# Performance work log

Measured on AMD Instinct MI355X. Metric: run time of the kernel, lower is better.

## Reference

```python
import jax, jax.numpy as jnp
import numpy as np

N, F, H, D, E, G = 50000, 64, 4, 64, 800000, 64
NEG_SLOPE = 0.2


def setup_inputs() -> dict:
    key = jax.random.key(0)
    ks = jax.random.split(key, 10)
    return {
        "x": jax.random.normal(ks[0], (N, F), jnp.float32),
        "mask": jax.random.uniform(ks[1], (N, F), jnp.float32),
        "edge_index": jax.random.randint(ks[2], (2, E), 0, N, jnp.int64),
        "batch_idx": jnp.sort(jax.random.randint(ks[3], (N,), 0, G, jnp.int64)),
        "W_gat": jax.random.normal(ks[4], (H * D, F), jnp.float32) * 0.05,
        "att_src": jax.random.normal(ks[5], (H, D), jnp.float32) * 0.05,
        "att_dst": jax.random.normal(ks[6], (H, D), jnp.float32) * 0.05,
        "bias_gat": jax.random.normal(ks[7], (H * D,), jnp.float32) * 0.05,
        "W_lin": jax.random.normal(ks[8], (D, H * D), jnp.float32) * 0.05,
        "b_lin": jax.random.normal(ks[9], (D,), jnp.float32) * 0.05,
    }


def reference(x, mask, edge_index, batch_idx, W_gat, att_src, att_dst, bias_gat, W_lin, b_lin):
    n = x.shape[0]
    row, col = edge_index[0], edge_index[1]

    # ---- get_mask(mask, edge_index, hops=1): scatter_add(mask[col] -> row), threshold
    m = jax.ops.segment_sum(mask[col], row, num_segments=n)
    m = (m > 0).astype(x.dtype)  # [N, F]

    # ---- GATConv(x, edge_index): add self loops (PyG default)
    loop = jnp.arange(n, dtype=edge_index.dtype)
    src = jnp.concatenate([edge_index[0], loop])  # source j
    dst = jnp.concatenate([edge_index[1], loop])  # target i

    xw = (x @ W_gat.T).reshape(n, H, D)  # per-head projection [N,H,D]
    a_s = jnp.einsum("nhd,hd->nh", xw, att_src)  # [N,H]
    a_d = jnp.einsum("nhd,hd->nh", xw, att_dst)
    e = jax.nn.leaky_relu(a_s[src] + a_d[dst], NEG_SLOPE)  # [E+N, H]

    # segment softmax over incoming edges of each destination node
    emax = jax.ops.segment_max(e, dst, num_segments=n)  # [N,H]
    ex = jnp.exp(e - emax[dst])
    denom = jax.ops.segment_sum(ex, dst, num_segments=n)
    alpha = ex / (denom[dst] + 1e-16)  # [E+N, H]

    out = jax.ops.segment_sum(alpha[:, :, None] * xw[src], dst, num_segments=n)
    out = out.reshape(n, H * D) + bias_gat  # concat heads + bias

    # ---- mask expand to heads and fuse: x = linear(x * mask)
    mexp = jnp.broadcast_to(m[:, None, :], (n, H, F)).reshape(n, H * F)
    out = (out * mexp) @ W_lin.T + b_lin  # [N, D]

    # ---- GraphSizeNorm: divide by sqrt(#nodes in each graph)
    deg = jax.ops.segment_sum(jnp.ones((n,), x.dtype), batch_idx, num_segments=G)
    inv_sqrt = jnp.where(deg > 0, deg, 1.0) ** -0.5
    out = out * inv_sqrt[batch_idx][:, None]
    return out
```

## Files before the change

kernel.cpp:

```cpp
#include <hip/hip_runtime.h>
#include <cstdint>
#include <math.h>

constexpr float NEG_SLOPE = 0.2f;

__device__ __forceinline__ float lrelu(float v) { return v > 0.0f ? v : NEG_SLOPE * v; }

__device__ __forceinline__ unsigned short f2bf(float f) {
    uint32_t u = __float_as_uint(f);
    uint32_t r = (u + 0x7fffu + ((u >> 16) & 1u)) >> 16;
    return (unsigned short)r;
}
__device__ __forceinline__ float bf2f(unsigned short v) { return __uint_as_float((uint32_t)v << 16); }
__device__ __forceinline__ float bflo(uint32_t v) { return __uint_as_float(v << 16); }
__device__ __forceinline__ float bfhi(uint32_t v) { return __uint_as_float(v & 0xffff0000u); }

typedef short bf16x8 __attribute__((ext_vector_type(8)));
typedef float f32x4 __attribute__((ext_vector_type(4)));

__global__ void k_init(const float* __restrict__ mask,
                       unsigned long long* __restrict__ mbits,
                       unsigned long long* __restrict__ magg,
                       int* __restrict__ deg, int* __restrict__ startg, int N)
{
    if (blockIdx.x == 0 && threadIdx.x < 64) startg[threadIdx.x] = N;
    int wid  = (blockIdx.x * blockDim.x + threadIdx.x) >> 6;
    int lane = threadIdx.x & 63;
    if (wid >= N) return;
    float v = mask[(size_t)wid * 64 + lane];
    unsigned long long b = __ballot(v > 0.0f);
    if (lane == 0) { mbits[wid] = b; magg[wid] = 0ULL; deg[wid] = 0; }
}

__global__ void k_deg(const int* __restrict__ ei, int* __restrict__ deg, int E)
{
    int e = blockIdx.x * blockDim.x + threadIdx.x;
    if (e >= E) return;
    atomicAdd(deg + ei[E + e], 1);
}

__launch_bounds__(256)
__global__ void k_att2(const float* __restrict__ x, const float* __restrict__ Wg,
                       const float* __restrict__ att_s, const float* __restrict__ att_d,
                       float* __restrict__ a_s, float* __restrict__ a_d, int N)
{
    __shared__ float vs_l[256];
    __shared__ float vd_l[256];
    int tid = threadIdx.x;
    {
        int h = tid >> 6, k = tid & 63;
        float s = 0.f, d = 0.f;
        for (int dd = 0; dd < 64; ++dd) {
            float w = Wg[(size_t)(h * 64 + dd) * 64 + k];
            s += w * att_s[h * 64 + dd];
            d += w * att_d[h * 64 + dd];
        }
        vs_l[tid] = s; vd_l[tid] = d;
    }
    __syncthreads();
    int i = blockIdx.x * 256 + tid;
    if (i >= N) return;
    const float4* xr = (const float4*)(x + (size_t)i * 64);
    float s0=0,s1=0,s2=0,s3=0, d0=0,d1=0,d2=0,d3=0;
    #pragma unroll
    for (int q = 0; q < 16; ++q) {
        float4 xv = xr[q];
        float4 a0 = *(const float4*)&vs_l[4*q];
        float4 a1 = *(const float4*)&vs_l[64 + 4*q];
        float4 a2 = *(const float4*)&vs_l[128 + 4*q];
        float4 a3 = *(const float4*)&vs_l[192 + 4*q];
        float4 c0 = *(const float4*)&vd_l[4*q];
        float4 c1 = *(const float4*)&vd_l[64 + 4*q];
        float4 c2 = *(const float4*)&vd_l[128 + 4*q];
        float4 c3 = *(const float4*)&vd_l[192 + 4*q];
        s0 += xv.x*a0.x + xv.y*a0.y + xv.z*a0.z + xv.w*a0.w;
        s1 += xv.x*a1.x + xv.y*a1.y + xv.z*a1.z + xv.w*a1.w;
        s2 += xv.x*a2.x + xv.y*a2.y + xv.z*a2.z + xv.w*a2.w;
        s3 += xv.x*a3.x + xv.y*a3.y + xv.z*a3.z + xv.w*a3.w;
        d0 += xv.x*c0.x + xv.y*c0.y + xv.z*c0.z + xv.w*c0.w;
        d1 += xv.x*c1.x + xv.y*c1.y + xv.z*c1.z + xv.w*c1.w;
        d2 += xv.x*c2.x + xv.y*c2.y + xv.z*c2.z + xv.w*c2.w;
        d3 += xv.x*c3.x + xv.y*c3.y + xv.z*c3.z + xv.w*c3.w;
    }
    *(float4*)&a_s[(size_t)i * 4] = make_float4(s0, s1, s2, s3);
    *(float4*)&a_d[(size_t)i * 4] = make_float4(d0, d1, d2, d3);
}

__launch_bounds__(256)
__global__ void k_gemm1m(const float* __restrict__ x, const float* __restrict__ Wg,
                         const int* __restrict__ batch_idx,
                         uint32_t* __restrict__ xwp, int* __restrict__ startg, int N)
{
    __shared__ __align__(16) uint32_t AsH[2048];
    __shared__ __align__(16) uint32_t AsL[2048];
    __shared__ __align__(16) uint32_t BsH[8192];
    const int tid = threadIdx.x;
    const int r0  = blockIdx.x * 64;

    for (int idx = tid; idx < 2048; idx += 256) {
        int r = idx >> 5, k2 = idx & 31;
        float2 v = make_float2(0.f, 0.f);
        if (r0 + r < N) v = *(const float2*)&x[(size_t)(r0 + r) * 64 + 2 * k2];
        unsigned short h0 = f2bf(v.x), h1 = f2bf(v.y);
        unsigned short l0 = f2bf(v.x - bf2f(h0)), l1 = f2bf(v.y - bf2f(h1));
        int di = (r * 32 + k2) ^ ((r & 7) << 2);
        AsH[di] = (uint32_t)h0 | ((uint32_t)h1 << 16);
        AsL[di] = (uint32_t)l0 | ((uint32_t)l1 << 16);
    }
    for (int idx = tid; idx < 8192; idx += 256) {
        int c = idx >> 5, k2 = idx & 31;
        float2 v = *(const float2*)&Wg[(size_t)c * 64 + 2 * k2];
        int di = (c * 32 + k2) ^ ((c & 7) << 2);
        BsH[di] = (uint32_t)f2bf(v.x) | ((uint32_t)f2bf(v.y) << 16);
    }
    if (tid < 64 && (r0 + tid) < N) {
        int i = r0 + tid;
        int b = batch_idx[i];
        int pb = (i > 0) ? batch_idx[i - 1] : -1;
        if (b != pb) startg[b] = i;
    }
    __syncthreads();

    const int lane = tid & 63;
    const int wv   = tid >> 6;
    const int rl   = lane & 15;
    const int kg   = lane >> 4;
    const int ct0  = (wv & 1) * 2 + (wv >> 1) * 8;
    const int swz  = (rl & 7) << 2;

    f32x4 acc[4][4];
    #pragma unroll
    for (int r = 0; r < 4; ++r)
        #pragma unroll
        for (int cs = 0; cs < 4; ++cs) acc[r][cs] = (f32x4){0.f, 0.f, 0.f, 0.f};

    #pragma unroll
    for (int ks = 0; ks < 2; ++ks) {
        bf16x8 aH[4], aL[4], bH[4];
        #pragma unroll
        for (int r = 0; r < 4; ++r) {
            int ui = (((r * 16 + rl) * 32) + ks * 16 + kg * 4) ^ swz;
            aH[r] = *(const bf16x8*)&AsH[ui];
            aL[r] = *(const bf16x8*)&AsL[ui];
        }
        #pragma unroll
        for (int cs = 0; cs < 4; ++cs) {
            int ct = ct0 + (cs & 1) + (cs >> 1) * 4;
            int ui = (((ct * 16 + rl) * 32) + ks * 16 + kg * 4) ^ swz;
            bH[cs] = *(const bf16x8*)&BsH[ui];
        }
        #pragma unroll
        for (int r = 0; r < 4; ++r)
            #pragma unroll
            for (int cs = 0; cs < 4; ++cs) {
                acc[r][cs] = __builtin_amdgcn_mfma_f32_16x16x32_bf16(aH[r], bH[cs], acc[r][cs], 0, 0, 0);
                acc[r][cs] = __builtin_amdgcn_mfma_f32_16x16x32_bf16(aL[r], bH[cs], acc[r][cs], 0, 0, 0);
            }
    }

    #pragma unroll
    for (int r = 0; r < 4; ++r) {
        #pragma unroll
        for (int reg = 0; reg < 4; ++reg) {
            int row = r0 + r * 16 + kg * 4 + reg;
            if (row < N) {
                #pragma unroll
                for (int p = 0; p < 2; ++p) {
                    int c_lo = (ct0 + p) * 16 + rl;
                    int wrd  = ((c_lo >> 7) << 6) | (c_lo & 63);
                    uint32_t lo = f2bf(acc[r][p][reg]);
                    uint32_t hi = f2bf(acc[r][p + 2][reg]);
                    xwp[(size_t)row * 128 + wrd] = lo | (hi << 16);
                }
            }
        }
    }
}

__global__ void k_scan1(const int* __restrict__ deg, int* __restrict__ off,
                        int* __restrict__ bsum, int N)
{
    __shared__ int s[256];
    int t = threadIdx.x;
    int i = blockIdx.x * 256 + t;
    int v = (i < N) ? deg[i] : 0;
    s[t] = v; __syncthreads();
    for (int o = 1; o < 256; o <<= 1) {
        int u = (t >= o) ? s[t - o] : 0;
        __syncthreads();
        s[t] += u;
        __syncthreads();
    }
    int incl = s[t];
    if (i < N) off[i] = incl - v;
    if (t == 255) bsum[blockIdx.x] = incl;
}

__global__ void k_scan2(const int* __restrict__ bsum, int* __restrict__ bpre,
                        int* __restrict__ off, const int* __restrict__ startg,
                        float* __restrict__ invs, int NB, int N)
{
    __shared__ int s[256];
    int t = threadIdx.x;
    int v = (t < NB) ? bsum[t] : 0;
    s[t] = v; __syncthreads();
    for (int o = 1; o < 256; o <<= 1) {
        int u = (t >= o) ? s[t - o] : 0;
        __syncthreads();
        s[t] += u;
        __syncthreads();
    }
    if (t < NB) bpre[t] = s[t] - v;
    if (t == 255) off[N] = s[255];
    if (t < 64) {
        int st = startg[t];
        int en = N;
        for (int g2 = t + 1; g2 < 64; ++g2) en = min(en, startg[g2]);
        int d = en - st;
        float dv = (d > 0) ? (float)d : 1.0f;
        invs[t] = 1.0f / sqrtf(dv);
    }
}

__global__ void k_scan3(int* __restrict__ off, int* __restrict__ cursor,
                        const int* __restrict__ bpre, int N)
{
    int i = blockIdx.x * blockDim.x + threadIdx.x;
    if (i >= N) return;
    int v = off[i] + bpre[blockIdx.x];
    off[i] = v;
    cursor[i] = v;
}

__global__ void k_fill(const int* __restrict__ ei, int* __restrict__ cursor,
                       int* __restrict__ csr,
                       const unsigned long long* __restrict__ mbits,
                       unsigned long long* __restrict__ magg, int E)
{
    int e = blockIdx.x * blockDim.x + threadIdx.x;
    if (e >= E) return;
    int r = ei[e];
    int c = ei[E + e];
    unsigned long long b = mbits[c];
    if ((magg[r] & b) != b) atomicOr(magg + r, b);
    int pos = atomicAdd(cursor + c, 1);
    csr[pos] = r;
}

__launch_bounds__(256)
__global__ void k_main6(const uint32_t* __restrict__ xwp,
                        const float* __restrict__ a_s,
                        const float* __restrict__ a_d,
                        const int* __restrict__ off,
                        const int* __restrict__ csr,
                        const unsigned long long* __restrict__ magg,
                        const float* __restrict__ bias,
                        float* __restrict__ tb, int N)
{
    __shared__ __align__(16) uint32_t su[4][64];
    __shared__ __align__(16) float2 e01s[4][64];
    __shared__ __align__(16) float2 e23s[4][64];

    const int lane = threadIdx.x & 63;
    const int wv   = threadIdx.x >> 6;
    const int wid  = blockIdx.x * 4 + wv;
    const int nw   = gridDim.x * 4;
    const int hp   = lane >> 5;
    const int d0   = (lane & 31) * 2;

    const uint2* xw2 = (const uint2*)xwp;
    const float2 bsL = *(const float2*)&bias[hp * 128 + d0];
    const float2 bsH = *(const float2*)&bias[hp * 128 + 64 + d0];
    const float2* ep = hp ? e23s[wv] : e01s[wv];

    for (int i = wid; i < N; i += nw) {
        const int beg = off[i], end = off[i + 1];
        const float4 adv = *(const float4*)(a_d + (size_t)i * 4);
        const float4 asv = *(const float4*)(a_s + (size_t)i * 4);
        const float ex0 = __expf(lrelu(asv.x + adv.x));
        const float ex1 = __expf(lrelu(asv.y + adv.y));
        const float ex2 = __expf(lrelu(asv.z + adv.z));
        const float ex3 = __expf(lrelu(asv.w + adv.w));

        const uint2 sv = xw2[(size_t)i * 64 + lane];
        const float wls = hp ? ex2 : ex0;
        const float whs = hp ? ex3 : ex1;
        float accL0 = wls * bflo(sv.x), accH0 = whs * bfhi(sv.x);
        float accL1 = wls * bflo(sv.y), accH1 = whs * bfhi(sv.y);
        float s0 = 0.f, s1 = 0.f, s2 = 0.f, s3 = 0.f;

        for (int kc = beg; kc < end; kc += 64) {
            const int cnt = min(64, end - kc);
            uint32_t sreg = 0; float e0 = 0.f, e1 = 0.f, e2 = 0.f, e3 = 0.f;
            if (lane < cnt) {
                sreg = csr[kc + lane];
                const float4 g = *(const float4*)(a_s + (size_t)sreg * 4);
                e0 = __expf(lrelu(g.x + adv.x));
                e1 = __expf(lrelu(g.y + adv.y));
                e2 = __expf(lrelu(g.z + adv.z));
                e3 = __expf(lrelu(g.w + adv.w));
            }
            s0 += e0; s1 += e1; s2 += e2; s3 += e3;
            su[wv][lane]   = sreg;
            e01s[wv][lane] = make_float2(e0, e1);
            e23s[wv][lane] = make_float2(e2, e3);

            int j = 0;
            for (; j + 8 <= cnt; j += 8) {
                uint4 sq0 = *(const uint4*)&su[wv][j];
                uint4 sq1 = *(const uint4*)&su[wv][j + 4];
                float2 w0 = ep[j],   w1 = ep[j+1], w2 = ep[j+2], w3 = ep[j+3];
                float2 w4 = ep[j+4], w5 = ep[j+5], w6 = ep[j+6], w7 = ep[j+7];
                uint2 v0 = xw2[(size_t)sq0.x * 64 + lane];
                uint2 v1 = xw2[(size_t)sq0.y * 64 + lane];
                uint2 v2 = xw2[(size_t)sq0.z * 64 + lane];
                uint2 v3 = xw2[(size_t)sq0.w * 64 + lane];
                uint2 v4 = xw2[(size_t)sq1.x * 64 + lane];
                uint2 v5 = xw2[(size_t)sq1.y * 64 + lane];
                uint2 v6 = xw2[(size_t)sq1.z * 64 + lane];
                uint2 v7 = xw2[(size_t)sq1.w * 64 + lane];
                accL0 += w0.x * bflo(v0.x); accH0 += w0.y * bfhi(v0.x);
                accL1 += w0.x * bflo(v0.y); accH1 += w0.y * bfhi(v0.y);
                accL0 += w1.x * bflo(v1.x); accH0 += w1.y * bfhi(v1.x);
                accL1 += w1.x * bflo(v1.y); accH1 += w1.y * bfhi(v1.y);
                accL0 += w2.x * bflo(v2.x); accH0 += w2.y * bfhi(v2.x);
                accL1 += w2.x * bflo(v2.y); accH1 += w2.y * bfhi(v2.y);
                accL0 += w3.x * bflo(v3.x); accH0 += w3.y * bfhi(v3.x);
                accL1 += w3.x * bflo(v3.y); accH1 += w3.y * bfhi(v3.y);
                accL0 += w4.x * bflo(v4.x); accH0 += w4.y * bfhi(v4.x);
                accL1 += w4.x * bflo(v4.y); accH1 += w4.y * bfhi(v4.y);
                accL0 += w5.x * bflo(v5.x); accH0 += w5.y * bfhi(v5.x);
                accL1 += w5.x * bflo(v5.y); accH1 += w5.y * bfhi(v5.y);
                accL0 += w6.x * bflo(v6.x); accH0 += w6.y * bfhi(v6.x);
                accL1 += w6.x * bflo(v6.y); accH1 += w6.y * bfhi(v6.y);
                accL0 += w7.x * bflo(v7.x); accH0 += w7.y * bfhi(v7.x);
                accL1 += w7.x * bflo(v7.y); accH1 += w7.y * bfhi(v7.y);
            }
            for (; j + 4 <= cnt; j += 4) {
                uint4 sq = *(const uint4*)&su[wv][j];
                float2 wA = ep[j], wB = ep[j+1], wC = ep[j+2], wD = ep[j+3];
                uint2 vA = xw2[(size_t)sq.x * 64 + lane];
                uint2 vB = xw2[(size_t)sq.y * 64 + lane];
                uint2 vC = xw2[(size_t)sq.z * 64 + lane];
                uint2 vD = xw2[(size_t)sq.w * 64 + lane];
                accL0 += wA.x * bflo(vA.x); accH0 += wA.y * bfhi(vA.x);
                accL1 += wA.x * bflo(vA.y); accH1 += wA.y * bfhi(vA.y);
                accL0 += wB.x * bflo(vB.x); accH0 += wB.y * bfhi(vB.x);
                accL1 += wB.x * bflo(vB.y); accH1 += wB.y * bfhi(vB.y);
                accL0 += wC.x * bflo(vC.x); accH0 += wC.y * bfhi(vC.x);
                accL1 += wC.x * bflo(vC.y); accH1 += wC.y * bfhi(vC.y);
                accL0 += wD.x * bflo(vD.x); accH0 += wD.y * bfhi(vD.x);
                accL1 += wD.x * bflo(vD.y); accH1 += wD.y * bfhi(vD.y);
            }
            for (; j < cnt; ++j) {
                uint32_t s = su[wv][j];
                float2 wE = ep[j];
                uint2 v = xw2[(size_t)s * 64 + lane];
                accL0 += wE.x * bflo(v.x); accH0 += wE.y * bfhi(v.x);
                accL1 += wE.x * bflo(v.y); accH1 += wE.y * bfhi(v.y);
            }
        }
        #pragma unroll
        for (int o = 1; o < 64; o <<= 1) {
            s0 += __shfl_xor(s0, o); s1 += __shfl_xor(s1, o);
            s2 += __shfl_xor(s2, o); s3 += __shfl_xor(s3, o);
        }
        s0 += ex0; s1 += ex1; s2 += ex2; s3 += ex3;
        const float slo = hp ? s2 : s0;
        const float shi = hp ? s3 : s1;
        const float rlo = 1.0f / (slo + 1e-16f);
        const float rhi = 1.0f / (shi + 1e-16f);

        const unsigned long long mb = magg[i];
        const float m0 = (float)((mb >> d0) & 1ULL);
        const float m1 = (float)((mb >> (d0 + 1)) & 1ULL);
        float2 oL = make_float2((accL0 * rlo + bsL.x) * m0, (accL1 * rlo + bsL.y) * m1);
        float2 oH = make_float2((accH0 * rhi + bsH.x) * m0, (accH1 * rhi + bsH.y) * m1);
        *(float2*)&tb[(size_t)i * 256 + hp * 128 + d0]      = oL;
        *(float2*)&tb[(size_t)i * 256 + hp * 128 + 64 + d0] = oH;
    }
}

__launch_bounds__(256)
__global__ void k_gemm2m(const float* __restrict__ tb, const float* __restrict__ Wl,
                         const float* __restrict__ bl,
                         const int* __restrict__ batch_idx, const float* __restrict__ invs,
                         float* __restrict__ out, int N)
{
    __shared__ __align__(16) uint32_t AH[2048];
    __shared__ __align__(16) uint32_t AL[2048];
    __shared__ __align__(16) uint32_t BH[2048];
    __shared__ __align__(16) uint32_t BL[2048];
    const int tid = threadIdx.x;
    const int r0  = blockIdx.x * 64;
    const int lane = tid & 63;
    const int wv   = tid >> 6;
    const int rl   = lane & 15;
    const int kg   = lane >> 4;
    const int swz  = (rl & 7) << 2;

    f32x4 acc[4];
    #pragma unroll
    for (int r = 0; r < 4; ++r) acc[r] = (f32x4){0.f, 0.f, 0.f, 0.f};

    for (int kc = 0; kc < 4; ++kc) {
        if (kc) __syncthreads();
        for (int idx = tid; idx < 2048; idx += 256) {
            int r = idx >> 5, k2 = idx & 31;
            float2 v = make_float2(0.f, 0.f);
            if (r0 + r < N) v = *(const float2*)&tb[(size_t)(r0 + r) * 256 + kc * 64 + 2 * k2];
            unsigned short h0 = f2bf(v.x), h1 = f2bf(v.y);
            unsigned short l0 = f2bf(v.x - bf2f(h0)), l1 = f2bf(v.y - bf2f(h1));
            int di = (r * 32 + k2) ^ ((r & 7) << 2);
            AH[di] = (uint32_t)h0 | ((uint32_t)h1 << 16);
            AL[di] = (uint32_t)l0 | ((uint32_t)l1 << 16);
        }
        for (int idx = tid; idx < 2048; idx += 256) {
            int c = idx >> 5, k2 = idx & 31;
            float2 v = *(const float2*)&Wl[(size_t)c * 256 + kc * 64 + 2 * k2];
            unsigned short h0 = f2bf(v.x), h1 = f2bf(v.y);
            unsigned short l0 = f2bf(v.x - bf2f(h0)), l1 = f2bf(v.y - bf2f(h1));
            int di = (c * 32 + k2) ^ ((c & 7) << 2);
            BH[di] = (uint32_t)h0 | ((uint32_t)h1 << 16);
            BL[di] = (uint32_t)l0 | ((uint32_t)l1 << 16);
        }
        __syncthreads();

        #pragma unroll
        for (int ks = 0; ks < 2; ++ks) {
            int uib = ((wv * 16 + rl) * 32 + ks * 16 + kg * 4) ^ swz;
            bf16x8 bHf = *(const bf16x8*)&BH[uib];
            bf16x8 bLf = *(const bf16x8*)&BL[uib];
            #pragma unroll
            for (int r = 0; r < 4; ++r) {
                int ui = ((r * 16 + rl) * 32 + ks * 16 + kg * 4) ^ swz;
                bf16x8 aHf = *(const bf16x8*)&AH[ui];
                bf16x8 aLf = *(const bf16x8*)&AL[ui];
                acc[r] = __builtin_amdgcn_mfma_f32_16x16x32_bf16(aHf, bHf, acc[r], 0, 0, 0);
                acc[r] = __builtin_amdgcn_mfma_f32_16x16x32_bf16(aHf, bLf, acc[r], 0, 0, 0);
                acc[r] = __builtin_amdgcn_mfma_f32_16x16x32_bf16(aLf, bHf, acc[r], 0, 0, 0);
            }
        }
    }

    const int col = wv * 16 + rl;
    const float blc = bl[col];
    #pragma unroll
    for (int r = 0; r < 4; ++r) {
        #pragma unroll
        for (int reg = 0; reg < 4; ++reg) {
            int row = r0 + r * 16 + kg * 4 + reg;
            if (row < N) {
                float sc = invs[batch_idx[row]];
                out[(size_t)row * 64 + col] = (acc[r][reg] + blc) * sc;
            }
        }
    }
}

extern "C" void kernel_launch(void* const* d_in, const int* in_sizes, int n_in,
                              void* d_out, int out_size, void* d_ws, size_t ws_size,
                              hipStream_t stream)
{
    const float* x      = (const float*)d_in[0];
    const float* mask   = (const float*)d_in[1];
    const int*   ei     = (const int*)d_in[2];
    const int*   batch  = (const int*)d_in[3];
    const float* Wg     = (const float*)d_in[4];
    const float* att_s  = (const float*)d_in[5];
    const float* att_d  = (const float*)d_in[6];
    const float* bias_g = (const float*)d_in[7];
    const float* Wl     = (const float*)d_in[8];
    const float* bl     = (const float*)d_in[9];
    float* out = (float*)d_out;

    const int N = in_sizes[0] / 64;
    const int E = in_sizes[2] / 2;

    char* w = (char*)d_ws;
    auto alloc = [&](size_t bytes) { char* p = w; w += (bytes + 255) & ~(size_t)255; return p; };
    uint32_t* xwp  = (uint32_t*)alloc((size_t)N * 128 * 4);
    float* tbuf  = (float*)alloc((size_t)N * 256 * 4);
    float* a_s   = (float*)alloc((size_t)N * 4 * 4);
    float* a_d   = (float*)alloc((size_t)N * 4 * 4);
    unsigned long long* mbits = (unsigned long long*)alloc((size_t)N * 8);
    unsigned long long* magg  = (unsigned long long*)alloc((size_t)N * 8);
    int* deg    = (int*)alloc((size_t)N * 4);
    int* off    = (int*)alloc((size_t)(N + 1) * 4);
    int* cursor = (int*)alloc((size_t)N * 4);
    int* csr    = (int*)alloc((size_t)E * 4);
    int* bsum   = (int*)alloc(256 * 4);
    int* bpre   = (int*)alloc(256 * 4);
    int* startg = (int*)alloc(64 * 4);
    float* invs = (float*)alloc(64 * 4);

    int nbN4  = (N + 3) / 4;
    int nb256 = (N + 255) / 256;

    k_init<<<nbN4, 256, 0, stream>>>(mask, mbits, magg, deg, startg, N);
    k_deg<<<(E + 255) / 256, 256, 0, stream>>>(ei, deg, E);
    k_att2<<<nb256, 256, 0, stream>>>(x, Wg, att_s, att_d, a_s, a_d, N);
    k_gemm1m<<<(N + 63) / 64, 256, 0, stream>>>(x, Wg, batch, xwp, startg, N);
    k_scan1<<<nb256, 256, 0, stream>>>(deg, off, bsum, N);
    k_scan2<<<1, 256, 0, stream>>>(bsum, bpre, off, startg, invs, nb256, N);
    k_scan3<<<nb256, 256, 0, stream>>>(off, cursor, bpre, N);
    k_fill<<<(E + 255) / 256, 256, 0, stream>>>(ei, cursor, csr, mbits, magg, E);
    k_main6<<<2048, 256, 0, stream>>>(xwp, a_s, a_d, off, csr, magg, bias_g, tbuf, N);
    k_gemm2m<<<(N + 63) / 64, 256, 0, stream>>>(tbuf, Wl, bl, batch, invs, out, N);
}
```

Baseline: 243.5 us.

## Store attention output as bf16, fuse init kernels, drop softmax-sum shuffles

The GAT aggregation kernel now writes its per-node output as packed bf16 instead of fp32. This halves the intermediate buffer traffic and lets the second GEMM skip the hi/lo split of A and one of its three MFMAs. The zero-init of deg/magg/startg moves into the attention-score kernel, and the mask-ballot and degree-count kernels merge into one launch. The softmax denominators are now accumulated per lane from the shared weights, replacing the cross-lane shuffle reduction. The bf16 intermediate trades accuracy for bandwidth.

```diff
diff --git a/kernel.cpp b/kernel.cpp
--- a/kernel.cpp
+++ b/kernel.cpp
@@ -18,31 +18,12 @@
 typedef short bf16x8 __attribute__((ext_vector_type(8)));
 typedef float f32x4 __attribute__((ext_vector_type(4)));
 
-__global__ void k_init(const float* __restrict__ mask,
-                       unsigned long long* __restrict__ mbits,
-                       unsigned long long* __restrict__ magg,
-                       int* __restrict__ deg, int* __restrict__ startg, int N)
-{
-    if (blockIdx.x == 0 && threadIdx.x < 64) startg[threadIdx.x] = N;
-    int wid  = (blockIdx.x * blockDim.x + threadIdx.x) >> 6;
-    int lane = threadIdx.x & 63;
-    if (wid >= N) return;
-    float v = mask[(size_t)wid * 64 + lane];
-    unsigned long long b = __ballot(v > 0.0f);
-    if (lane == 0) { mbits[wid] = b; magg[wid] = 0ULL; deg[wid] = 0; }
-}
-
-__global__ void k_deg(const int* __restrict__ ei, int* __restrict__ deg, int E)
-{
-    int e = blockIdx.x * blockDim.x + threadIdx.x;
-    if (e >= E) return;
-    atomicAdd(deg + ei[E + e], 1);
-}
-
 __launch_bounds__(256)
-__global__ void k_att2(const float* __restrict__ x, const float* __restrict__ Wg,
-                       const float* __restrict__ att_s, const float* __restrict__ att_d,
-                       float* __restrict__ a_s, float* __restrict__ a_d, int N)
+__global__ void k_att2z(const float* __restrict__ x, const float* __restrict__ Wg,
+                        const float* __restrict__ att_s, const float* __restrict__ att_d,
+                        float* __restrict__ a_s, float* __restrict__ a_d,
+                        int* __restrict__ deg, unsigned long long* __restrict__ magg,
+                        int* __restrict__ startg, int N)
 {
     __shared__ float vs_l[256];
     __shared__ float vd_l[256];
@@ -57,9 +38,11 @@
         }
         vs_l[tid] = s; vd_l[tid] = d;
     }
+    if (blockIdx.x == 0 && tid < 64) startg[tid] = N;
     __syncthreads();
     int i = blockIdx.x * 256 + tid;
     if (i >= N) return;
+    deg[i] = 0; magg[i] = 0ULL;
     const float4* xr = (const float4*)(x + (size_t)i * 64);
     float s0=0,s1=0,s2=0,s3=0, d0=0,d1=0,d2=0,d3=0;
     #pragma unroll
@@ -86,6 +69,25 @@
     *(float4*)&a_d[(size_t)i * 4] = make_float4(d0, d1, d2, d3);
 }
 
+__global__ void k_maskdeg(const float* __restrict__ mask, const int* __restrict__ ei,
+                          unsigned long long* __restrict__ mbits, int* __restrict__ deg,
+                          int N, int E, int nbMask)
+{
+    int tid = threadIdx.x;
+    if ((int)blockIdx.x < nbMask) {
+        int wid  = (blockIdx.x * 256 + tid) >> 6;
+        int lane = tid & 63;
+        if (wid >= N) return;
+        float v = mask[(size_t)wid * 64 + lane];
+        unsigned long long b = __ballot(v > 0.0f);
+        if (lane == 0) mbits[wid] = b;
+    } else {
+        int e = (blockIdx.x - nbMask) * 256 + tid;
+        if (e >= E) return;
+        atomicAdd(deg + ei[E + e], 1);
+    }
+}
+
 __launch_bounds__(256)
 __global__ void k_gemm1m(const float* __restrict__ x, const float* __restrict__ Wg,
                          const int* __restrict__ batch_idx,
@@ -248,14 +250,14 @@
 }
 
 __launch_bounds__(256)
-__global__ void k_main6(const uint32_t* __restrict__ xwp,
+__global__ void k_main7(const uint32_t* __restrict__ xwp,
                         const float* __restrict__ a_s,
                         const float* __restrict__ a_d,
                         const int* __restrict__ off,
                         const int* __restrict__ csr,
                         const unsigned long long* __restrict__ magg,
                         const float* __restrict__ bias,
-                        float* __restrict__ tb, int N)
+                        uint32_t* __restrict__ tbp, int N)
 {
     __shared__ __align__(16) uint32_t su[4][64];
     __shared__ __align__(16) float2 e01s[4][64];
@@ -287,7 +289,7 @@
         const float whs = hp ? ex3 : ex1;
         float accL0 = wls * bflo(sv.x), accH0 = whs * bfhi(sv.x);
         float accL1 = wls * bflo(sv.y), accH1 = whs * bfhi(sv.y);
-        float s0 = 0.f, s1 = 0.f, s2 = 0.f, s3 = 0.f;
+        float sL = 0.f, sH = 0.f;
 
         for (int kc = beg; kc < end; kc += 64) {
             const int cnt = min(64, end - kc);
@@ -300,7 +302,6 @@
                 e2 = __expf(lrelu(g.z + adv.z));
                 e3 = __expf(lrelu(g.w + adv.w));
             }
-            s0 += e0; s1 += e1; s2 += e2; s3 += e3;
             su[wv][lane]   = sreg;
             e01s[wv][lane] = make_float2(e0, e1);
             e23s[wv][lane] = make_float2(e2, e3);
@@ -319,6 +320,8 @@
                 uint2 v5 = xw2[(size_t)sq1.y * 64 + lane];
                 uint2 v6 = xw2[(size_t)sq1.z * 64 + lane];
                 uint2 v7 = xw2[(size_t)sq1.w * 64 + lane];
+                sL += w0.x + w1.x + w2.x + w3.x + w4.x + w5.x + w6.x + w7.x;
+                sH += w0.y + w1.y + w2.y + w3.y + w4.y + w5.y + w6.y + w7.y;
                 accL0 += w0.x * bflo(v0.x); accH0 += w0.y * bfhi(v0.x);
                 accL1 += w0.x * bflo(v0.y); accH1 += w0.y * bfhi(v0.y);
                 accL0 += w1.x * bflo(v1.x); accH0 += w1.y * bfhi(v1.x);
@@ -343,6 +346,8 @@
                 uint2 vB = xw2[(size_t)sq.y * 64 + lane];
                 uint2 vC = xw2[(size_t)sq.z * 64 + lane];
                 uint2 vD = xw2[(size_t)sq.w * 64 + lane];
+                sL += wA.x + wB.x + wC.x + wD.x;
+                sH += wA.y + wB.y + wC.y + wD.y;
                 accL0 += wA.x * bflo(vA.x); accH0 += wA.y * bfhi(vA.x);
                 accL1 += wA.x * bflo(vA.y); accH1 += wA.y * bfhi(vA.y);
                 accL0 += wB.x * bflo(vB.x); accH0 += wB.y * bfhi(vB.x);
@@ -356,39 +361,31 @@
                 uint32_t s = su[wv][j];
                 float2 wE = ep[j];
                 uint2 v = xw2[(size_t)s * 64 + lane];
+                sL += wE.x; sH += wE.y;
                 accL0 += wE.x * bflo(v.x); accH0 += wE.y * bfhi(v.x);
                 accL1 += wE.x * bflo(v.y); accH1 += wE.y * bfhi(v.y);
             }
         }
-        #pragma unroll
-        for (int o = 1; o < 64; o <<= 1) {
-            s0 += __shfl_xor(s0, o); s1 += __shfl_xor(s1, o);
-            s2 += __shfl_xor(s2, o); s3 += __shfl_xor(s3, o);
-        }
-        s0 += ex0; s1 += ex1; s2 += ex2; s3 += ex3;
-        const float slo = hp ? s2 : s0;
-        const float shi = hp ? s3 : s1;
-        const float rlo = 1.0f / (slo + 1e-16f);
-        const float rhi = 1.0f / (shi + 1e-16f);
+        const float rlo = 1.0f / (sL + wls + 1e-16f);
+        const float rhi = 1.0f / (sH + whs + 1e-16f);
 
         const unsigned long long mb = magg[i];
         const float m0 = (float)((mb >> d0) & 1ULL);
         const float m1 = (float)((mb >> (d0 + 1)) & 1ULL);
-        float2 oL = make_float2((accL0 * rlo + bsL.x) * m0, (accL1 * rlo + bsL.y) * m1);
-        float2 oH = make_float2((accH0 * rhi + bsH.x) * m0, (accH1 * rhi + bsH.y) * m1);
-        *(float2*)&tb[(size_t)i * 256 + hp * 128 + d0]      = oL;
-        *(float2*)&tb[(size_t)i * 256 + hp * 128 + 64 + d0] = oH;
+        float oL0 = (accL0 * rlo + bsL.x) * m0, oL1 = (accL1 * rlo + bsL.y) * m1;
+        float oH0 = (accH0 * rhi + bsH.x) * m0, oH1 = (accH1 * rhi + bsH.y) * m1;
+        tbp[(size_t)i * 128 + hp * 64 + (lane & 31)]      = (uint32_t)f2bf(oL0) | ((uint32_t)f2bf(oL1) << 16);
+        tbp[(size_t)i * 128 + hp * 64 + 32 + (lane & 31)] = (uint32_t)f2bf(oH0) | ((uint32_t)f2bf(oH1) << 16);
     }
 }
 
 __launch_bounds__(256)
-__global__ void k_gemm2m(const float* __restrict__ tb, const float* __restrict__ Wl,
+__global__ void k_gemm2m(const uint32_t* __restrict__ tbp, const float* __restrict__ Wl,
                          const float* __restrict__ bl,
                          const int* __restrict__ batch_idx, const float* __restrict__ invs,
                          float* __restrict__ out, int N)
 {
     __shared__ __align__(16) uint32_t AH[2048];
-    __shared__ __align__(16) uint32_t AL[2048];
     __shared__ __align__(16) uint32_t BH[2048];
     __shared__ __align__(16) uint32_t BL[2048];
     const int tid = threadIdx.x;
@@ -407,13 +404,9 @@
         if (kc) __syncthreads();
         for (int idx = tid; idx < 2048; idx += 256) {
             int r = idx >> 5, k2 = idx & 31;
-            float2 v = make_float2(0.f, 0.f);
-            if (r0 + r < N) v = *(const float2*)&tb[(size_t)(r0 + r) * 256 + kc * 64 + 2 * k2];
-            unsigned short h0 = f2bf(v.x), h1 = f2bf(v.y);
-            unsigned short l0 = f2bf(v.x - bf2f(h0)), l1 = f2bf(v.y - bf2f(h1));
-            int di = (r * 32 + k2) ^ ((r & 7) << 2);
-            AH[di] = (uint32_t)h0 | ((uint32_t)h1 << 16);
-            AL[di] = (uint32_t)l0 | ((uint32_t)l1 << 16);
+            uint32_t v = 0;
+            if (r0 + r < N) v = tbp[(size_t)(r0 + r) * 128 + kc * 32 + k2];
+            AH[(r * 32 + k2) ^ ((r & 7) << 2)] = v;
         }
         for (int idx = tid; idx < 2048; idx += 256) {
             int c = idx >> 5, k2 = idx & 31;
@@ -435,10 +428,8 @@
             for (int r = 0; r < 4; ++r) {
                 int ui = ((r * 16 + rl) * 32 + ks * 16 + kg * 4) ^ swz;
                 bf16x8 aHf = *(const bf16x8*)&AH[ui];
-                bf16x8 aLf = *(const bf16x8*)&AL[ui];
                 acc[r] = __builtin_amdgcn_mfma_f32_16x16x32_bf16(aHf, bHf, acc[r], 0, 0, 0);
                 acc[r] = __builtin_amdgcn_mfma_f32_16x16x32_bf16(aHf, bLf, acc[r], 0, 0, 0);
-                acc[r] = __builtin_amdgcn_mfma_f32_16x16x32_bf16(aLf, bHf, acc[r], 0, 0, 0);
             }
         }
     }
@@ -480,7 +471,7 @@
     char* w = (char*)d_ws;
     auto alloc = [&](size_t bytes) { char* p = w; w += (bytes + 255) & ~(size_t)255; return p; };
     uint32_t* xwp  = (uint32_t*)alloc((size_t)N * 128 * 4);
-    float* tbuf  = (float*)alloc((size_t)N * 256 * 4);
+    uint32_t* tbp  = (uint32_t*)alloc((size_t)N * 128 * 4);
     float* a_s   = (float*)alloc((size_t)N * 4 * 4);
     float* a_d   = (float*)alloc((size_t)N * 4 * 4);
     unsigned long long* mbits = (unsigned long long*)alloc((size_t)N * 8);
@@ -495,16 +486,16 @@
     float* invs = (float*)alloc(64 * 4);
 
     int nbN4  = (N + 3) / 4;
+    int nbE   = (E + 255) / 256;
     int nb256 = (N + 255) / 256;
 
-    k_init<<<nbN4, 256, 0, stream>>>(mask, mbits, magg, deg, startg, N);
-    k_deg<<<(E + 255) / 256, 256, 0, stream>>>(ei, deg, E);
-    k_att2<<<nb256, 256, 0, stream>>>(x, Wg, att_s, att_d, a_s, a_d, N);
+    k_att2z<<<nb256, 256, 0, stream>>>(x, Wg, att_s, att_d, a_s, a_d, deg, magg, startg, N);
+    k_maskdeg<<<nbN4 + nbE, 256, 0, stream>>>(mask, ei, mbits, deg, N, E, nbN4);
     k_gemm1m<<<(N + 63) / 64, 256, 0, stream>>>(x, Wg, batch, xwp, startg, N);
     k_scan1<<<nb256, 256, 0, stream>>>(deg, off, bsum, N);
     k_scan2<<<1, 256, 0, stream>>>(bsum, bpre, off, startg, invs, nb256, N);
     k_scan3<<<nb256, 256, 0, stream>>>(off, cursor, bpre, N);
-    k_fill<<<(E + 255) / 256, 256, 0, stream>>>(ei, cursor, csr, mbits, magg, E);
-    k_main6<<<2048, 256, 0, stream>>>(xwp, a_s, a_d, off, csr, magg, bias_g, tbuf, N);
-    k_gemm2m<<<(N + 63) / 64, 256, 0, stream>>>(tbuf, Wl, bl, batch, invs, out, N);
-}
+    k_fill<<<nbE, 256, 0, stream>>>(ei, cursor, csr, mbits, magg, E);
+    k_main7<<<2048, 256, 0, stream>>>(xwp, a_s, a_d, off, csr, magg, bias_g, tbp, N);
+    k_gemm2m<<<(N + 63) / 64, 256, 0, stream>>>(tbp, Wl, bl, batch, invs, out, N);
+}
```

After: 234.6 us. -3.6%, faster.
